# Kernel tuning notes

Hardware: AMD Instinct MI355X
Metric: run time of the kernel (lower is better)

Reference implementation:

```python
import jax, jax.numpy as jnp
import numpy as np

B, T, HID, MC, L, NCLS = 256, 128, 64, 30, 2, 100


def _flow(x, t, fW0, fb0, fW1, fb1, fW2, fb2, ftw):
    # Continuous affine coupling flow (stribor). x: [..., S, HID], t: [..., S, 1]
    hid = x.shape[-1]
    base = (jnp.arange(hid) < hid // 2).astype(x.dtype)  # ordered_0 mask
    for l in range(fW0.shape[0]):
        m = base if l % 2 == 0 else 1.0 - base
        z = x * m
        a = jnp.tanh(jnp.concatenate([z, t], -1) @ fW0[l] + fb0[l])
        a = jnp.tanh(a @ fW1[l] + fb1[l])
        ss = a @ fW2[l] + fb2[l]                      # [..., 2*hid]
        scale, shift = jnp.split(ss, 2, -1)
        t_scale, t_shift = jnp.split(jnp.tanh(t * ftw[l]), 2, -1)  # TimeTanh
        x = z + (1.0 - m) * (x * jnp.exp(scale * t_scale) + shift * t_shift)
    return x


def setup_inputs() -> dict:
    key = jax.random.key(0)
    ks = jax.random.split(key, 12)
    n = lambda k, s, sc=0.1: jax.random.normal(k, s, dtype=jnp.float32) * sc
    return {
        "times": jax.random.uniform(ks[0], (B, T, 1), dtype=jnp.float32),
        "marks": jax.random.randint(ks[1], (B, T, 1), 0, NCLS),
        "mask": jnp.ones((B, T, 1), jnp.float32),
        "u": jax.random.uniform(ks[2], (T, MC, 1), dtype=jnp.float32),
        "emb": n(ks[3], (NCLS, HID), 1.0),
        "fW0": n(ks[4], (L, HID + 1, HID)),
        "fb0": jnp.zeros((L, HID), jnp.float32),
        "fW1": n(ks[5], (L, HID, HID)),
        "fb1": jnp.zeros((L, HID), jnp.float32),
        "fW2": n(ks[6], (L, HID, 2 * HID)),
        "fb2": jnp.zeros((L, 2 * HID), jnp.float32),
        "ftw": n(ks[7], (L, 2 * HID), 1.0),
        "Wi": n(ks[8], (HID, 1)),
        "bi": jnp.zeros((1,), jnp.float32),
        "W_ih": n(ks[9], (4 * HID, 1 + HID)),
        "W_hh": n(ks[10], (4 * HID, HID)),
        "b_ih": jnp.zeros((4 * HID,), jnp.float32),
        "b_hh": jnp.zeros((4 * HID,), jnp.float32),
    }


def reference(times, marks, mask, u, emb, fW0, fb0, fW1, fb1, fW2, fb2, ftw,
              Wi, bi, W_ih, W_hh, b_ih, b_hh):
    Bn, Tn, _ = times.shape
    hid = emb.shape[1]
    mc = u.shape[1]
    marks_e = emb[marks[..., 0]]      # [B,T,hid]
    m1 = marks_e[:, 1]                # source uses marks[:, 1] every step (faithful)
    inten = lambda x: jax.nn.softplus(x @ Wi + bi)

    def step(carry, xs):
        h, c = carry                  # h,c: [B,hid]
        t, u_i = xs                   # t: [B,1], u_i: [mc,1]
        t3 = t[:, None, :]            # [B,1,1]
        ts = u_i[None] * t3           # [B,mc,1] MC time samples in [0,t)
        xb = jnp.broadcast_to(h[:, None, :], (Bn, mc, hid))
        path = _flow(xb, ts, fW0, fb0, fW1, fb1, fW2, fb2, ftw)   # [B,mc,hid]
        integral = inten(path).mean(1, keepdims=True) * t3        # [B,1,1]
        h2 = _flow(h[:, None, :], t3, fW0, fb0, fW1, fb1, fW2, fb2, ftw)  # [B,1,hid]
        lam = inten(h2)                                           # [B,1,1]
        gates = jnp.concatenate([t, m1], -1) @ W_ih.T + b_ih + h2[:, 0] @ W_hh.T + b_hh
        ig, fg, gg, og = jnp.split(gates, 4, -1)
        c_n = jax.nn.sigmoid(fg) * c + jax.nn.sigmoid(ig) * jnp.tanh(gg)
        h_n = jax.nn.sigmoid(og) * jnp.tanh(c_n)
        nll = -jnp.log(lam[:, 0]) + integral[:, 0]                # [B,1]
        return (h_n, c_n), (h2[:, 0], nll)

    h0 = jnp.zeros((Bn, hid), times.dtype)
    (_, _), (hidden, nll) = jax.lax.scan(step, (h0, h0), (jnp.swapaxes(times, 0, 1), u))
    hidden = jnp.swapaxes(hidden, 0, 1)                           # [B,T,hid]
    loss = (jnp.swapaxes(nll, 0, 1)[:, :, :] * mask[..., 0][..., None]).sum() / mask.sum()
    return loss, hidden
```

## Files before the change

kernel.cpp:

```cpp
#include <hip/hip_runtime.h>
#include <hip/hip_bf16.h>
#include <math.h>

#define Bn   256
#define Tn   128
#define HID  64
#define MCn  30

typedef __attribute__((ext_vector_type(8))) short bf16x8;
typedef __attribute__((ext_vector_type(4))) float f32x4;

__device__ __forceinline__ float rcp_(float x) { return __builtin_amdgcn_rcpf(x); }
__device__ __forceinline__ float tanhf_(float x) {
    float e = __expf(-2.0f * x);
    return __builtin_fmaf(2.0f, rcp_(1.0f + e), -1.0f);
}
__device__ __forceinline__ float sigmoidf_(float x) {
    return rcp_(1.0f + __expf(-x));
}
__device__ __forceinline__ float softplusf_(float z) {
    float e = __expf(-fabsf(z));
    return fmaxf(z, 0.0f) + __logf(1.0f + e);
}
__device__ __forceinline__ unsigned short f2b(float f) {
    union { float f; unsigned u; } v; v.f = f;
    unsigned r = v.u + 0x7FFF + ((v.u >> 16) & 1);
    return (unsigned short)(r >> 16);
}
__device__ __forceinline__ unsigned pk2(float a, float b) {
    union { __hip_bfloat162 h2; unsigned u; } cv;
    cv.h2 = __float22bfloat162_rn(make_float2(a, b));
    return cv.u;
}

extern "C" __global__ __launch_bounds__(256)
void prep_kernel(const int* __restrict__ marks, const float* __restrict__ mask,
                 const float* __restrict__ emb, const float* __restrict__ fW0,
                 const float* __restrict__ fW1, const float* __restrict__ fW2,
                 const float* __restrict__ fb0, const float* __restrict__ fb1,
                 const float* __restrict__ fb2, const float* __restrict__ ftw,
                 const float* __restrict__ Wi, const float* __restrict__ W_ih,
                 const float* __restrict__ W_hh,
                 const float* __restrict__ b_ih, const float* __restrict__ b_hh,
                 float* __restrict__ gc, float* __restrict__ invd,
                 float* __restrict__ parv, unsigned short* __restrict__ parwb,
                 float* __restrict__ seqw1T, float* __restrict__ seqw2T,
                 float* __restrict__ whh260)
{
    __shared__ float red[4];
    const int blk = blockIdx.x, tid = threadIdx.x;
    if (blk < Bn) {
        const int mark = marks[blk * Tn + 1];
        const float* er = emb + mark * HID;
        const float* wr = W_ih + tid * 65 + 1;
        float acc = b_ih[tid] + b_hh[tid];
        #pragma unroll
        for (int k = 0; k < HID; k++) acc += er[k] * wr[k];
        gc[blk * 256 + tid] = acc;
    } else if (blk == Bn) {
        float s = 0.f;
        for (int i = tid; i < Bn * Tn; i += 256) s += mask[i];
        #pragma unroll
        for (int off = 32; off >= 1; off >>= 1) s += __shfl_xor(s, off, 64);
        if ((tid & 63) == 0) red[tid >> 6] = s;
        __syncthreads();
        if (tid == 0) invd[0] = 1.0f / (red[0] + red[1] + red[2] + red[3]);
    } else if (blk == Bn + 1) {
        if (tid < 128) {
            int l = tid >> 6, m = tid & 63;
            parv[tid]       = fb0[tid];
            parv[128 + tid] = fW0[(l * 65 + 64) * 64 + m];
            parv[256 + tid] = fb1[tid];
            int act = 32 * (1 - l);
            parv[384 + tid] = fb2[l * 128 + act + (m & 31) + 64 * (m >> 5)];
        }
        if (tid < 64) {
            int l = tid >> 5, i2 = tid & 31, act = 32 * (1 - l);
            parv[512 + tid] = ftw[l * 128 + act + i2];
            parv[576 + tid] = ftw[l * 128 + 64 + act + i2];
            parv[640 + tid] = Wi[tid];
            parv[704 + tid] = 0.f;
        }
    } else if (blk == Bn + 2) {
        for (int i = tid; i < 5120; i += 256) {
            int k = i % 40, m = (i / 40) & 63, l = i / 2560;
            float v = (k < 32) ? fW0[(l * 65 + 32 * l + k) * 64 + m] : 0.f;
            parwb[i] = f2b(v);
        }
    } else if (blk == Bn + 3) {
        for (int i = tid; i < 9216; i += 256) {
            int k = i % 72, m = (i / 72) & 63, l = i / 4608;
            float v = (k < 64) ? fW1[(l * 64 + k) * 64 + m] : 0.f;
            parwb[5120 + i] = f2b(v);
        }
    } else if (blk == Bn + 4) {
        for (int i = tid; i < 9216; i += 256) {
            int k = i % 72, m = (i / 72) & 63, l = i / 4608;
            int act = 32 * (1 - l);
            float v = (k < 64) ? fW2[(l * 64 + k) * 128 + act + (m & 31) + 64 * (m >> 5)] : 0.f;
            parwb[14336 + i] = f2b(v);
        }
    } else if (blk == Bn + 5) {
        for (int i = tid; i < 8704; i += 256) {
            int k = i % 68, j = (i / 68) & 63, l = i / 4352;
            seqw1T[i] = (k < 64) ? fW1[(l * 64 + k) * 64 + j] : 0.f;
        }
    } else if (blk == Bn + 6) {
        for (int i = tid; i < 8704; i += 256) {
            int k = i % 68, j = (i / 68) & 63, l = i / 4352;
            int act = 32 * (1 - l);
            seqw2T[i] = (k < 64) ?
                fW2[(l * 64 + k) * 128 + act + (j & 31) + 64 * (j >> 5)] : 0.f;
        }
    } else {
        for (int i = tid; i < 16640; i += 256) {
            int j = i / 260, rem = i % 260, k = rem >> 2, r = rem & 3;
            whh260[i] = (k < 64) ? W_hh[(r * 64 + j) * 64 + k] : 0.f;
        }
    }
}

extern "C" __global__ __launch_bounds__(64, 1)
void seq_kernel(const float* __restrict__ times, const float* __restrict__ mask,
                const float* __restrict__ fW0, const float* __restrict__ fb0,
                const float* __restrict__ fb1, const float* __restrict__ fb2,
                const float* __restrict__ ftw, const float* __restrict__ Wi,
                const float* __restrict__ bi, const float* __restrict__ W_ih,
                const float* __restrict__ gc, const float* __restrict__ seqw1T,
                const float* __restrict__ invd,
                float* __restrict__ h_carry, float* __restrict__ out)
{
    const int j = threadIdx.x;
    const int b = blockIdx.x;

    extern __shared__ float smem[];
    float* w1l  = smem;
    float* w2l  = smem + 8704;
    float* whhl = smem + 17408;
    float* tl   = smem + 34048;
    float* ml   = smem + 34176;
    float* xl   = smem + 34304;
    float* al   = smem + 34368;
    float* ssl  = smem + 34432;

    {
        const float4* s = (const float4*)seqw1T;
        float4* d = (float4*)smem;
        for (int i = j; i < 8512; i += 64) d[i] = s[i];
    }
    tl[j] = times[b * Tn + j];       tl[j + 64] = times[b * Tn + 64 + j];
    ml[j] = mask[b * Tn + j];        ml[j + 64] = mask[b * Tn + 64 + j];

    float w0c[2][32], w0tc[2], b0c[2], b1c[2], b2c[2], ftsc[2], ftsh[2];
    #pragma unroll
    for (int l = 0; l < 2; l++) {
        #pragma unroll
        for (int kk = 0; kk < 32; kk++)
            w0c[l][kk] = fW0[(l * 65 + 32 * l + kk) * 64 + j];
        w0tc[l] = fW0[(l * 65 + 64) * 64 + j];
        b0c[l]  = fb0[l * 64 + j];
        b1c[l]  = fb1[l * 64 + j];
        const int act = 32 * (1 - l);
        b2c[l]  = fb2[l * 128 + act + (j & 31) + 64 * (j >> 5)];
        ftsc[l] = ftw[l * 128 + j];
        ftsh[l] = ftw[l * 128 + 64 + j];
    }
    const float wij = Wi[j];
    const float bi0 = bi[0];
    float wih0[4], gcr[4];
    #pragma unroll
    for (int r = 0; r < 4; r++) {
        wih0[r] = W_ih[(r * 64 + j) * 65];
        gcr[r]  = gc[b * 256 + r * 64 + j];
    }
    const float idn = invd[0];

    float h = 0.f, c = 0.f, nllacc = 0.f;
    for (int t = 0; t < Tn; t++) {
        const float tb = tl[t];
        float tscv[2], tshv[2];
        #pragma unroll
        for (int l = 0; l < 2; l++) {
            tscv[l] = tanhf_(tb * ftsc[l]);
            tshv[l] = tanhf_(tb * ftsh[l]);
        }
        h_carry[(b * Tn + t) * 64 + j] = h;
        float x = h;
        xl[j] = x;
        #pragma unroll
        for (int l = 0; l < 2; l++) {
            const int kb  = 32 * l;
            const int act = 32 * (1 - l);
            float p0 = b0c[l] + tb * w0tc[l], p1 = 0.f, p2 = 0.f, p3 = 0.f;
            {
                const float4* xv4 = (const float4*)(xl + kb);
                #pragma unroll
                for (int k4 = 0; k4 < 8; k4++) {
                    float4 xv = xv4[k4];
                    p0 += xv.x * w0c[l][4 * k4 + 0];
                    p1 += xv.y * w0c[l][4 * k4 + 1];
                    p2 += xv.z * w0c[l][4 * k4 + 2];
                    p3 += xv.w * w0c[l][4 * k4 + 3];
                }
            }
            al[j] = tanhf_((p0 + p1) + (p2 + p3));
            p0 = b1c[l]; p1 = p2 = p3 = 0.f;
            {
                const float4* av4 = (const float4*)al;
                const float*  wp  = w1l + (l * 64 + j) * 68;
                #pragma unroll
                for (int k4 = 0; k4 < 16; k4++) {
                    float4 av = av4[k4];
                    float4 wv = *(const float4*)(wp + 4 * k4);
                    p0 += av.x * wv.x;
                    p1 += av.y * wv.y;
                    p2 += av.z * wv.z;
                    p3 += av.w * wv.w;
                }
            }
            al[j] = tanhf_((p0 + p1) + (p2 + p3));
            p0 = b2c[l]; p1 = p2 = p3 = 0.f;
            {
                const float4* av4 = (const float4*)al;
                const float*  wp  = w2l + (l * 64 + j) * 68;
                #pragma unroll
                for (int k4 = 0; k4 < 16; k4++) {
                    float4 av = av4[k4];
                    float4 wv = *(const float4*)(wp + 4 * k4);
                    p0 += av.x * wv.x;
                    p1 += av.y * wv.y;
                    p2 += av.z * wv.z;
                    p3 += av.w * wv.w;
                }
            }
            ssl[j] = (p0 + p1) + (p2 + p3);
            const int idx = (j - act) & 31;
            const float scl = ssl[idx];
            const float shf = ssl[idx + 32];
            const float xa  = x * __expf(scl * tscv[l]) + shf * tshv[l];
            const bool active = (l == 0) ? (j >= 32) : (j < 32);
            x = active ? xa : x;
            xl[j] = x;
        }
        out[1 + (b * Tn + t) * 64 + j] = x;
        float v = x * wij;
        #pragma unroll
        for (int off = 32; off >= 1; off >>= 1) v += __shfl_xor(v, off, 64);
        nllacc += -__logf(softplusf_(v + bi0)) * ml[t];
        float g0 = gcr[0] + tb * wih0[0];
        float g1 = gcr[1] + tb * wih0[1];
        float g2 = gcr[2] + tb * wih0[2];
        float g3 = gcr[3] + tb * wih0[3];
        {
            const float*  wr_base = whhl + j * 260;
            const float4* hv4 = (const float4*)xl;
            #pragma unroll
            for (int k4 = 0; k4 < 16; k4++) {
                float4 hv = hv4[k4];
                const float* wr = wr_base + 16 * k4;
                float4 wa = *(const float4*)(wr);
                float4 wb = *(const float4*)(wr + 4);
                float4 wc = *(const float4*)(wr + 8);
                float4 wd = *(const float4*)(wr + 12);
                g0 += hv.x * wa.x; g1 += hv.x * wa.y; g2 += hv.x * wa.z; g3 += hv.x * wa.w;
                g0 += hv.y * wb.x; g1 += hv.y * wb.y; g2 += hv.y * wb.z; g3 += hv.y * wb.w;
                g0 += hv.z * wc.x; g1 += hv.z * wc.y; g2 += hv.z * wc.z; g3 += hv.z * wc.w;
                g0 += hv.w * wd.x; g1 += hv.w * wd.y; g2 += hv.w * wd.z; g3 += hv.w * wd.w;
            }
        }
        c = sigmoidf_(g1) * c + sigmoidf_(g0) * tanhf_(g2);
        h = sigmoidf_(g3) * tanhf_(c);
    }
    if (j == 0) atomicAdd(out, nllacc * idn);
}

extern "C" __global__ __launch_bounds__(256, 2)
void par_kernel(const float* __restrict__ times, const float* __restrict__ mask,
                const float* __restrict__ u, const float* __restrict__ bi,
                const float* __restrict__ invd, const float* __restrict__ parv,
                const unsigned short* __restrict__ parwb,
                const float* __restrict__ h_carry, float* __restrict__ pp)
{
    __shared__ __align__(16) unsigned short sact[128 * 72];
    __shared__ __align__(16) unsigned short sxk1[128 * 40];
    __shared__ __align__(16) unsigned short sx0b[4 * 40];
    __shared__ float pr[4];

    const int tid = threadIdx.x, lane = tid & 63, w = tid >> 6;
    const int quad = lane >> 4, l15 = lane & 15;

    const int q = blockIdx.x * 4 + w;
    const int t = q >> 8, b = q & 255;
    const float tb = times[b * Tn + t];
    const float* hrow = h_carry + (b * Tn + t) * 64;
    if (lane < 32) sx0b[w * 40 + lane] = f2b(hrow[lane]);

    float tsv[2], sclf[2];
    {
        const float base = tb * (1.0f / 30.0f) * invd[0] * mask[b * Tn + t];
        #pragma unroll
        for (int nt = 0; nt < 2; nt++) {
            int mc = nt * 16 + l15;
            bool val = (mc < 30);
            tsv[nt]  = val ? u[t * MCn + mc] * tb : 0.f;
            sclf[nt] = val ? base : 0.f;
        }
    }
    f32x4 xr[2][4];
    #pragma unroll
    for (int mt = 0; mt < 4; mt++) {
        f32x4 v = *(const f32x4*)(hrow + mt * 16 + quad * 4);
        xr[0][mt] = v; xr[1][mt] = v;
    }
    const int srow = w * 32;

    #pragma unroll
    for (int l = 0; l < 2; l++) {
        const unsigned short* wA1 = parwb + l * 2560;
        const unsigned short* wA2 = parwb + 5120 + l * 4608;
        const unsigned short* wA3 = parwb + 14336 + l * 4608;
        f32x4 c1[4][2];
        if (l == 0) {
            bf16x8 bb = *(const bf16x8*)(sx0b + w * 40 + quad * 8);
            #pragma unroll
            for (int mt = 0; mt < 4; mt++) {
                bf16x8 af = *(const bf16x8*)(wA1 + (mt * 16 + l15) * 40 + quad * 8);
                f32x4 z = {0.f, 0.f, 0.f, 0.f};
                c1[mt][0] = __builtin_amdgcn_mfma_f32_16x16x32_bf16(af, bb, z, 0, 0, 0);
                c1[mt][1] = c1[mt][0];
            }
        } else {
            bf16x8 bf[2];
            #pragma unroll
            for (int nt = 0; nt < 2; nt++)
                bf[nt] = *(const bf16x8*)(sxk1 + (srow + nt * 16 + l15) * 40 + quad * 8);
            #pragma unroll
            for (int mt = 0; mt < 4; mt++) {
                bf16x8 af = *(const bf16x8*)(wA1 + (mt * 16 + l15) * 40 + quad * 8);
                #pragma unroll
                for (int nt = 0; nt < 2; nt++) {
                    f32x4 z = {0.f, 0.f, 0.f, 0.f};
                    c1[mt][nt] = __builtin_amdgcn_mfma_f32_16x16x32_bf16(af, bf[nt], z, 0, 0, 0);
                }
            }
        }
        #pragma unroll
        for (int mt = 0; mt < 4; mt++) {
            f32x4 b0r = *(const f32x4*)(parv + 0   + l * 64 + mt * 16 + quad * 4);
            f32x4 w0r = *(const f32x4*)(parv + 128 + l * 64 + mt * 16 + quad * 4);
            #pragma unroll
            for (int nt = 0; nt < 2; nt++) {
                float v0 = tanhf_(c1[mt][nt][0] + b0r[0] + tsv[nt] * w0r[0]);
                float v1 = tanhf_(c1[mt][nt][1] + b0r[1] + tsv[nt] * w0r[1]);
                float v2 = tanhf_(c1[mt][nt][2] + b0r[2] + tsv[nt] * w0r[2]);
                float v3 = tanhf_(c1[mt][nt][3] + b0r[3] + tsv[nt] * w0r[3]);
                uint2 pk; pk.x = pk2(v0, v1); pk.y = pk2(v2, v3);
                *(uint2*)(sact + (srow + nt * 16 + l15) * 72 + mt * 16 + quad * 4) = pk;
            }
        }
        f32x4 cc[4][2];
        #pragma unroll
        for (int mt = 0; mt < 4; mt++)
            #pragma unroll
            for (int nt = 0; nt < 2; nt++) cc[mt][nt] = (f32x4){0.f, 0.f, 0.f, 0.f};
        #pragma unroll
        for (int kt = 0; kt < 2; kt++) {
            bf16x8 bf[2];
            #pragma unroll
            for (int nt = 0; nt < 2; nt++)
                bf[nt] = *(const bf16x8*)(sact + (srow + nt * 16 + l15) * 72 + kt * 32 + quad * 8);
            #pragma unroll
            for (int mt = 0; mt < 4; mt++) {
                bf16x8 af = *(const bf16x8*)(wA2 + (mt * 16 + l15) * 72 + kt * 32 + quad * 8);
                #pragma unroll
                for (int nt = 0; nt < 2; nt++)
                    cc[mt][nt] = __builtin_amdgcn_mfma_f32_16x16x32_bf16(af, bf[nt], cc[mt][nt], 0, 0, 0);
            }
        }
        #pragma unroll
        for (int mt = 0; mt < 4; mt++) {
            f32x4 b1r = *(const f32x4*)(parv + 256 + l * 64 + mt * 16 + quad * 4);
            #pragma unroll
            for (int nt = 0; nt < 2; nt++) {
                float v0 = tanhf_(cc[mt][nt][0] + b1r[0]);
                float v1 = tanhf_(cc[mt][nt][1] + b1r[1]);
                float v2 = tanhf_(cc[mt][nt][2] + b1r[2]);
                float v3 = tanhf_(cc[mt][nt][3] + b1r[3]);
                uint2 pk; pk.x = pk2(v0, v1); pk.y = pk2(v2, v3);
                *(uint2*)(sact + (srow + nt * 16 + l15) * 72 + mt * 16 + quad * 4) = pk;
            }
        }
        f32x4 ssf[4][2];
        #pragma unroll
        for (int mt = 0; mt < 4; mt++)
            #pragma unroll
            for (int nt = 0; nt < 2; nt++) ssf[mt][nt] = (f32x4){0.f, 0.f, 0.f, 0.f};
        #pragma unroll
        for (int kt = 0; kt < 2; kt++) {
            bf16x8 bf[2];
            #pragma unroll
            for (int nt = 0; nt < 2; nt++)
                bf[nt] = *(const bf16x8*)(sact + (srow + nt * 16 + l15) * 72 + kt * 32 + quad * 8);
            #pragma unroll
            for (int mt = 0; mt < 4; mt++) {
                bf16x8 af = *(const bf16x8*)(wA3 + (mt * 16 + l15) * 72 + kt * 32 + quad * 8);
                #pragma unroll
                for (int nt = 0; nt < 2; nt++)
                    ssf[mt][nt] = __builtin_amdgcn_mfma_f32_16x16x32_bf16(af, bf[nt], ssf[mt][nt], 0, 0, 0);
            }
        }
        #pragma unroll
        for (int mt2 = 0; mt2 < 2; mt2++) {
            f32x4 b2s = *(const f32x4*)(parv + 384 + l * 64 +      mt2 * 16 + quad * 4);
            f32x4 b2h = *(const f32x4*)(parv + 384 + l * 64 + 32 + mt2 * 16 + quad * 4);
            f32x4 fa  = *(const f32x4*)(parv + 512 + l * 32 + mt2 * 16 + quad * 4);
            f32x4 fb  = *(const f32x4*)(parv + 576 + l * 32 + mt2 * 16 + quad * 4);
            const int xm = (l == 0) ? (mt2 + 2) : mt2;
            #pragma unroll
            for (int nt = 0; nt < 2; nt++) {
                #pragma unroll
                for (int r = 0; r < 4; r++) {
                    float sc  = ssf[mt2][nt][r] + b2s[r];
                    float sh  = ssf[mt2 + 2][nt][r] + b2h[r];
                    float tsc = tanhf_(tsv[nt] * fa[r]);
                    float tsh = tanhf_(tsv[nt] * fb[r]);
                    float xv  = xr[nt][xm][r];
                    xr[nt][xm][r] = xv * __expf(sc * tsc) + sh * tsh;
                }
                if (l == 0) {
                    uint2 pk;
                    pk.x = pk2(xr[nt][xm][0], xr[nt][xm][1]);
                    pk.y = pk2(xr[nt][xm][2], xr[nt][xm][3]);
                    *(uint2*)(sxk1 + (srow + nt * 16 + l15) * 40 + mt2 * 16 + quad * 4) = pk;
                }
            }
        }
    }
    float contrib = 0.f;
    const float bi0 = bi[0];
    #pragma unroll
    for (int nt = 0; nt < 2; nt++) {
        float d0 = 0.f, d1 = 0.f;
        #pragma unroll
        for (int mt = 0; mt < 4; mt++) {
            f32x4 wi4 = *(const f32x4*)(parv + 640 + mt * 16 + quad * 4);
            d0 += xr[nt][mt][0] * wi4[0] + xr[nt][mt][2] * wi4[2];
            d1 += xr[nt][mt][1] * wi4[1] + xr[nt][mt][3] * wi4[3];
        }
        float d = d0 + d1;
        d += __shfl_xor(d, 16, 64);
        d += __shfl_xor(d, 32, 64);
        contrib += softplusf_(d + bi0) * sclf[nt];
    }
    if (quad != 0) contrib = 0.f;
    #pragma unroll
    for (int off = 1; off <= 8; off <<= 1) contrib += __shfl_xor(contrib, off, 64);
    if (l15 == 0 && quad == 0) pr[w] = contrib;
    __syncthreads();
    if (tid == 0) pp[blockIdx.x] = pr[0] + pr[1] + pr[2] + pr[3];
}

extern "C" __global__ __launch_bounds__(256)
void fin_kernel(const float* __restrict__ pp, float* __restrict__ out)
{
    __shared__ float r4[4];
    const int tid = threadIdx.x;
    float s = 0.f;
    for (int i = tid; i < (Bn * Tn) / 4; i += 256) s += pp[i];
    #pragma unroll
    for (int off = 32; off >= 1; off >>= 1) s += __shfl_xor(s, off, 64);
    if ((tid & 63) == 0) r4[tid >> 6] = s;
    __syncthreads();
    if (tid == 0) atomicAdd(out, r4[0] + r4[1] + r4[2] + r4[3]);
}

extern "C" void kernel_launch(void* const* d_in, const int* in_sizes, int n_in,
                              void* d_out, int out_size, void* d_ws, size_t ws_size,
                              hipStream_t stream)
{
    const float* times = (const float*)d_in[0];
    const int*   marks = (const int*)  d_in[1];
    const float* mask  = (const float*)d_in[2];
    const float* u     = (const float*)d_in[3];
    const float* emb   = (const float*)d_in[4];
    const float* fW0   = (const float*)d_in[5];
    const float* fb0   = (const float*)d_in[6];
    const float* fW1   = (const float*)d_in[7];
    const float* fb1   = (const float*)d_in[8];
    const float* fW2   = (const float*)d_in[9];
    const float* fb2   = (const float*)d_in[10];
    const float* ftw   = (const float*)d_in[11];
    const float* Wi    = (const float*)d_in[12];
    const float* bi    = (const float*)d_in[13];
    const float* W_ih  = (const float*)d_in[14];
    const float* W_hh  = (const float*)d_in[15];
    const float* b_ih  = (const float*)d_in[16];
    const float* b_hh  = (const float*)d_in[17];
    float* out = (float*)d_out;

    float* wsp     = (float*)d_ws;
    float* h_carry = wsp;
    float* gc      = h_carry + 2097152;
    float* invd    = gc + 65536;
    float* seqw1T  = invd + 4;
    float* seqw2T  = seqw1T + 8704;
    float* whh260  = seqw2T + 8704;
    float* parv    = whh260 + 16640;
    unsigned short* parwb = (unsigned short*)(parv + 768);
    float* pp      = (float*)(parwb + 23552);

    hipMemsetAsync(d_out, 0, sizeof(float), stream);

    const int SEQ_SMEM = 34496 * 4;
    hipFuncSetAttribute((const void*)seq_kernel,
                        hipFuncAttributeMaxDynamicSharedMemorySize, SEQ_SMEM);

    prep_kernel<<<Bn + 8, 256, 0, stream>>>(marks, mask, emb, fW0, fW1, fW2,
                                            fb0, fb1, fb2, ftw, Wi, W_ih, W_hh,
                                            b_ih, b_hh, gc, invd, parv, parwb,
                                            seqw1T, seqw2T, whh260);
    seq_kernel<<<Bn, 64, SEQ_SMEM, stream>>>(times, mask, fW0, fb0, fb1, fb2,
                                             ftw, Wi, bi, W_ih, gc, seqw1T,
                                             invd, h_carry, out);
    par_kernel<<<(Bn * Tn) / 4, 256, 0, stream>>>(
        times, mask, u, bi, invd, parv, parwb, h_carry, pp);
    fin_kernel<<<1, 256, 0, stream>>>(pp, out);
}
```

Baseline: 690.1 us.

## Fuse sequential LSTM scan with MC integral flow into one warp-specialized kernel

Merges seq_kernel, par_kernel and fin_kernel into one kernel of three waves per batch row. Wave 0 runs the serial flow+LSTM recurrence while waves 1-2 evaluate the Monte Carlo flow integral for the previous step's hidden state with MFMA, handing it over through a double-buffered shared hbuf. This removes the h_carry round trip through global memory, two kernel launches and the separate reduction, and hides the parallel work behind the serial chain. In exchange it adds a block barrier every timestep and runs the MC work on only 256 blocks instead of 8192.

```diff
diff --git a/kernel.cpp b/kernel.cpp
--- a/kernel.cpp
+++ b/kernel.cpp
@@ -120,18 +120,23 @@
     }
 }
 
-extern "C" __global__ __launch_bounds__(64, 1)
-void seq_kernel(const float* __restrict__ times, const float* __restrict__ mask,
-                const float* __restrict__ fW0, const float* __restrict__ fb0,
-                const float* __restrict__ fb1, const float* __restrict__ fb2,
-                const float* __restrict__ ftw, const float* __restrict__ Wi,
-                const float* __restrict__ bi, const float* __restrict__ W_ih,
-                const float* __restrict__ gc, const float* __restrict__ seqw1T,
-                const float* __restrict__ invd,
-                float* __restrict__ h_carry, float* __restrict__ out)
+extern "C" __global__ __launch_bounds__(192, 1)
+void fused_kernel(const float* __restrict__ times, const float* __restrict__ mask,
+                  const float* __restrict__ u,
+                  const float* __restrict__ fW0, const float* __restrict__ fb0,
+                  const float* __restrict__ fb1, const float* __restrict__ fb2,
+                  const float* __restrict__ ftw, const float* __restrict__ Wi,
+                  const float* __restrict__ bi, const float* __restrict__ W_ih,
+                  const float* __restrict__ gc, const float* __restrict__ seqw1T,
+                  const float* __restrict__ parv,
+                  const unsigned short* __restrict__ parwb,
+                  const float* __restrict__ invd, float* __restrict__ out)
 {
-    const int j = threadIdx.x;
-    const int b = blockIdx.x;
+    const int tid  = threadIdx.x;
+    const int lane = tid & 63;
+    const int w    = tid >> 6;
+    const int b    = blockIdx.x;
+    const int quad = lane >> 4, l15 = lane & 15;
 
     extern __shared__ float smem[];
     float* w1l  = smem;
@@ -142,336 +147,268 @@
     float* xl   = smem + 34304;
     float* al   = smem + 34368;
     float* ssl  = smem + 34432;
+    float* hbuf = smem + 34496;
+    float* pr   = smem + 34624;
+    unsigned short* csact = (unsigned short*)(smem + 34628);
+    unsigned short* csxk1 = csact + 2304;
+    unsigned short* csx0  = csxk1 + 1280;
 
     {
         const float4* s = (const float4*)seqw1T;
         float4* d = (float4*)smem;
-        for (int i = j; i < 8512; i += 64) d[i] = s[i];
+        for (int i = tid; i < 8512; i += 192) d[i] = s[i];
+        for (int i = tid; i < 128; i += 192) {
+            tl[i] = times[b * Tn + i];
+            ml[i] = mask[b * Tn + i];
+        }
     }
-    tl[j] = times[b * Tn + j];       tl[j + 64] = times[b * Tn + 64 + j];
-    ml[j] = mask[b * Tn + j];        ml[j + 64] = mask[b * Tn + 64 + j];
+
+    const float bi0 = bi[0];
+    const float idn = invd[0];
 
     float w0c[2][32], w0tc[2], b0c[2], b1c[2], b2c[2], ftsc[2], ftsh[2];
-    #pragma unroll
-    for (int l = 0; l < 2; l++) {
-        #pragma unroll
-        for (int kk = 0; kk < 32; kk++)
-            w0c[l][kk] = fW0[(l * 65 + 32 * l + kk) * 64 + j];
-        w0tc[l] = fW0[(l * 65 + 64) * 64 + j];
-        b0c[l]  = fb0[l * 64 + j];
-        b1c[l]  = fb1[l * 64 + j];
-        const int act = 32 * (1 - l);
-        b2c[l]  = fb2[l * 128 + act + (j & 31) + 64 * (j >> 5)];
-        ftsc[l] = ftw[l * 128 + j];
-        ftsh[l] = ftw[l * 128 + 64 + j];
-    }
-    const float wij = Wi[j];
-    const float bi0 = bi[0];
-    float wih0[4], gcr[4];
-    #pragma unroll
-    for (int r = 0; r < 4; r++) {
-        wih0[r] = W_ih[(r * 64 + j) * 65];
-        gcr[r]  = gc[b * 256 + r * 64 + j];
-    }
-    const float idn = invd[0];
-
+    float wih0[4], gcr[4], wij = 0.f;
     float h = 0.f, c = 0.f, nllacc = 0.f;
-    for (int t = 0; t < Tn; t++) {
-        const float tb = tl[t];
-        float tscv[2], tshv[2];
+    if (w == 0) {
         #pragma unroll
         for (int l = 0; l < 2; l++) {
-            tscv[l] = tanhf_(tb * ftsc[l]);
-            tshv[l] = tanhf_(tb * ftsh[l]);
-        }
-        h_carry[(b * Tn + t) * 64 + j] = h;
-        float x = h;
-        xl[j] = x;
+            #pragma unroll
+            for (int kk = 0; kk < 32; kk++)
+                w0c[l][kk] = fW0[(l * 65 + 32 * l + kk) * 64 + lane];
+            w0tc[l] = fW0[(l * 65 + 64) * 64 + lane];
+            b0c[l]  = fb0[l * 64 + lane];
+            b1c[l]  = fb1[l * 64 + lane];
+            const int act = 32 * (1 - l);
+            b2c[l]  = fb2[l * 128 + act + (lane & 31) + 64 * (lane >> 5)];
+            ftsc[l] = ftw[l * 128 + lane];
+            ftsh[l] = ftw[l * 128 + 64 + lane];
+        }
+        wij = Wi[lane];
         #pragma unroll
-        for (int l = 0; l < 2; l++) {
-            const int kb  = 32 * l;
-            const int act = 32 * (1 - l);
-            float p0 = b0c[l] + tb * w0tc[l], p1 = 0.f, p2 = 0.f, p3 = 0.f;
+        for (int r = 0; r < 4; r++) {
+            wih0[r] = W_ih[(r * 64 + lane) * 65];
+            gcr[r]  = gc[b * 256 + r * 64 + lane];
+        }
+    }
+    const int cw = w - 1;
+    unsigned short* myact = csact + cw * 1152;
+    unsigned short* myxk  = csxk1 + cw * 640;
+    unsigned short* myx0  = csx0  + cw * 40;
+    const int mc  = cw * 16 + l15;
+    const bool valmc = (w > 0) && (mc < MCn);
+    float wacc = 0.f;
+
+    __syncthreads();
+
+    for (int t = 0; t < Tn; t++) {
+        if (w == 0) hbuf[(t & 1) * 64 + lane] = h;
+        __syncthreads();
+
+        if (w == 0) {
+            const float tb = tl[t];
+            float tscv[2], tshv[2];
+            #pragma unroll
+            for (int l = 0; l < 2; l++) {
+                tscv[l] = tanhf_(tb * ftsc[l]);
+                tshv[l] = tanhf_(tb * ftsh[l]);
+            }
+            float x = h;
+            xl[lane] = x;
+            #pragma unroll
+            for (int l = 0; l < 2; l++) {
+                const int kb  = 32 * l;
+                const int act = 32 * (1 - l);
+                {
+                    float p0 = b0c[l] + tb * w0tc[l], p1 = 0.f, p2 = 0.f, p3 = 0.f;
+                    const float4* xv4 = (const float4*)(xl + kb);
+                    #pragma unroll
+                    for (int k4 = 0; k4 < 8; k4++) {
+                        float4 xv = xv4[k4];
+                        p0 += xv.x * w0c[l][4 * k4 + 0];
+                        p1 += xv.y * w0c[l][4 * k4 + 1];
+                        p2 += xv.z * w0c[l][4 * k4 + 2];
+                        p3 += xv.w * w0c[l][4 * k4 + 3];
+                    }
+                    al[lane] = tanhf_((p0 + p1) + (p2 + p3));
+                }
+                {
+                    float p0 = b1c[l], p1 = 0.f, p2 = 0.f, p3 = 0.f;
+                    const float4* av4 = (const float4*)al;
+                    const float*  wp  = w1l + (l * 64 + lane) * 68;
+                    #pragma unroll
+                    for (int k4 = 0; k4 < 16; k4++) {
+                        float4 av = av4[k4];
+                        float4 wv = *(const float4*)(wp + 4 * k4);
+                        p0 += av.x * wv.x; p1 += av.y * wv.y;
+                        p2 += av.z * wv.z; p3 += av.w * wv.w;
+                    }
+                    al[lane] = tanhf_((p0 + p1) + (p2 + p3));
+                }
+                {
+                    float p0 = b2c[l], p1 = 0.f, p2 = 0.f, p3 = 0.f;
+                    const float4* av4 = (const float4*)al;
+                    const float*  wp  = w2l + (l * 64 + lane) * 68;
+                    #pragma unroll
+                    for (int k4 = 0; k4 < 16; k4++) {
+                        float4 av = av4[k4];
+                        float4 wv = *(const float4*)(wp + 4 * k4);
+                        p0 += av.x * wv.x; p1 += av.y * wv.y;
+                        p2 += av.z * wv.z; p3 += av.w * wv.w;
+                    }
+                    ssl[lane] = (p0 + p1) + (p2 + p3);
+                }
+                const int idx = (lane - act) & 31;
+                const float scl = ssl[idx];
+                const float shf = ssl[idx + 32];
+                const float xa  = x * __expf(scl * tscv[l]) + shf * tshv[l];
+                const bool active = (l == 0) ? (lane >= 32) : (lane < 32);
+                x = active ? xa : x;
+                xl[lane] = x;
+            }
+            out[1 + (b * Tn + t) * 64 + lane] = x;
+            float v = x * wij;
+            #pragma unroll
+            for (int off = 32; off >= 1; off >>= 1) v += __shfl_xor(v, off, 64);
+            nllacc += -__logf(softplusf_(v + bi0)) * ml[t];
+            float g0 = gcr[0] + tb * wih0[0];
+            float g1 = gcr[1] + tb * wih0[1];
+            float g2 = gcr[2] + tb * wih0[2];
+            float g3 = gcr[3] + tb * wih0[3];
             {
-                const float4* xv4 = (const float4*)(xl + kb);
-                #pragma unroll
-                for (int k4 = 0; k4 < 8; k4++) {
-                    float4 xv = xv4[k4];
-                    p0 += xv.x * w0c[l][4 * k4 + 0];
-                    p1 += xv.y * w0c[l][4 * k4 + 1];
-                    p2 += xv.z * w0c[l][4 * k4 + 2];
-                    p3 += xv.w * w0c[l][4 * k4 + 3];
+                const float*  wr_base = whhl + lane * 260;
+                const float4* hv4 = (const float4*)xl;
+                #pragma unroll
+                for (int k4 = 0; k4 < 16; k4++) {
+                    float4 hv = hv4[k4];
+                    const float* wr = wr_base + 16 * k4;
+                    float4 wa = *(const float4*)(wr);
+                    float4 wb = *(const float4*)(wr + 4);
+                    float4 wc = *(const float4*)(wr + 8);
+                    float4 wd = *(const float4*)(wr + 12);
+                    g0 += hv.x * wa.x; g1 += hv.x * wa.y; g2 += hv.x * wa.z; g3 += hv.x * wa.w;
+                    g0 += hv.y * wb.x; g1 += hv.y * wb.y; g2 += hv.y * wb.z; g3 += hv.y * wb.w;
+                    g0 += hv.z * wc.x; g1 += hv.z * wc.y; g2 += hv.z * wc.z; g3 += hv.z * wc.w;
+                    g0 += hv.w * wd.x; g1 += hv.w * wd.y; g2 += hv.w * wd.z; g3 += hv.w * wd.w;
                 }
             }
-            al[j] = tanhf_((p0 + p1) + (p2 + p3));
-            p0 = b1c[l]; p1 = p2 = p3 = 0.f;
-            {
-                const float4* av4 = (const float4*)al;
-                const float*  wp  = w1l + (l * 64 + j) * 68;
-                #pragma unroll
-                for (int k4 = 0; k4 < 16; k4++) {
-                    float4 av = av4[k4];
-                    float4 wv = *(const float4*)(wp + 4 * k4);
-                    p0 += av.x * wv.x;
-                    p1 += av.y * wv.y;
-                    p2 += av.z * wv.z;
-                    p3 += av.w * wv.w;
+            c = sigmoidf_(g1) * c + sigmoidf_(g0) * tanhf_(g2);
+            h = sigmoidf_(g3) * tanhf_(c);
+        } else {
+            const float tb = tl[t];
+            const float ts   = valmc ? u[t * MCn + mc] * tb : 0.f;
+            const float sclf = valmc ? tb * (1.0f / 30.0f) * idn * ml[t] : 0.f;
+            const float* hb  = hbuf + (t & 1) * 64;
+            f32x4 xr[4];
+            #pragma unroll
+            for (int mt = 0; mt < 4; mt++)
+                xr[mt] = *(const f32x4*)(hb + mt * 16 + quad * 4);
+            if (lane < 32) myx0[lane] = f2b(hb[lane]);
+            #pragma unroll
+            for (int l = 0; l < 2; l++) {
+                const unsigned short* wA1 = parwb + l * 2560;
+                const unsigned short* wA2 = parwb + 5120 + l * 4608;
+                const unsigned short* wA3 = parwb + 14336 + l * 4608;
+                f32x4 c1[4];
+                {
+                    bf16x8 bfin = (l == 0) ? *(const bf16x8*)(myx0 + quad * 8)
+                                           : *(const bf16x8*)(myxk + l15 * 40 + quad * 8);
+                    #pragma unroll
+                    for (int mt = 0; mt < 4; mt++) {
+                        bf16x8 af = *(const bf16x8*)(wA1 + (mt * 16 + l15) * 40 + quad * 8);
+                        f32x4 z = {0.f, 0.f, 0.f, 0.f};
+                        c1[mt] = __builtin_amdgcn_mfma_f32_16x16x32_bf16(af, bfin, z, 0, 0, 0);
+                    }
+                }
+                #pragma unroll
+                for (int mt = 0; mt < 4; mt++) {
+                    f32x4 b0r = *(const f32x4*)(parv + 0   + l * 64 + mt * 16 + quad * 4);
+                    f32x4 w0r = *(const f32x4*)(parv + 128 + l * 64 + mt * 16 + quad * 4);
+                    float v0 = tanhf_(c1[mt][0] + b0r[0] + ts * w0r[0]);
+                    float v1 = tanhf_(c1[mt][1] + b0r[1] + ts * w0r[1]);
+                    float v2 = tanhf_(c1[mt][2] + b0r[2] + ts * w0r[2]);
+                    float v3 = tanhf_(c1[mt][3] + b0r[3] + ts * w0r[3]);
+                    uint2 pk; pk.x = pk2(v0, v1); pk.y = pk2(v2, v3);
+                    *(uint2*)(myact + l15 * 72 + mt * 16 + quad * 4) = pk;
+                }
+                f32x4 cc[4];
+                #pragma unroll
+                for (int mt = 0; mt < 4; mt++) cc[mt] = (f32x4){0.f, 0.f, 0.f, 0.f};
+                #pragma unroll
+                for (int kt = 0; kt < 2; kt++) {
+                    bf16x8 bfa = *(const bf16x8*)(myact + l15 * 72 + kt * 32 + quad * 8);
+                    #pragma unroll
+                    for (int mt = 0; mt < 4; mt++) {
+                        bf16x8 af = *(const bf16x8*)(wA2 + (mt * 16 + l15) * 72 + kt * 32 + quad * 8);
+                        cc[mt] = __builtin_amdgcn_mfma_f32_16x16x32_bf16(af, bfa, cc[mt], 0, 0, 0);
+                    }
+                }
+                #pragma unroll
+                for (int mt = 0; mt < 4; mt++) {
+                    f32x4 b1r = *(const f32x4*)(parv + 256 + l * 64 + mt * 16 + quad * 4);
+                    float v0 = tanhf_(cc[mt][0] + b1r[0]);
+                    float v1 = tanhf_(cc[mt][1] + b1r[1]);
+                    float v2 = tanhf_(cc[mt][2] + b1r[2]);
+                    float v3 = tanhf_(cc[mt][3] + b1r[3]);
+                    uint2 pk; pk.x = pk2(v0, v1); pk.y = pk2(v2, v3);
+                    *(uint2*)(myact + l15 * 72 + mt * 16 + quad * 4) = pk;
+                }
+                f32x4 ssf[4];
+                #pragma unroll
+                for (int mt = 0; mt < 4; mt++) ssf[mt] = (f32x4){0.f, 0.f, 0.f, 0.f};
+                #pragma unroll
+                for (int kt = 0; kt < 2; kt++) {
+                    bf16x8 bfa = *(const bf16x8*)(myact + l15 * 72 + kt * 32 + quad * 8);
+                    #pragma unroll
+                    for (int mt = 0; mt < 4; mt++) {
+                        bf16x8 af = *(const bf16x8*)(wA3 + (mt * 16 + l15) * 72 + kt * 32 + quad * 8);
+                        ssf[mt] = __builtin_amdgcn_mfma_f32_16x16x32_bf16(af, bfa, ssf[mt], 0, 0, 0);
+                    }
+                }
+                #pragma unroll
+                for (int mt2 = 0; mt2 < 2; mt2++) {
+                    f32x4 b2s = *(const f32x4*)(parv + 384 + l * 64 +      mt2 * 16 + quad * 4);
+                    f32x4 b2h = *(const f32x4*)(parv + 384 + l * 64 + 32 + mt2 * 16 + quad * 4);
+                    f32x4 fa  = *(const f32x4*)(parv + 512 + l * 32 + mt2 * 16 + quad * 4);
+                    f32x4 fb  = *(const f32x4*)(parv + 576 + l * 32 + mt2 * 16 + quad * 4);
+                    const int xm = (l == 0) ? (mt2 + 2) : mt2;
+                    #pragma unroll
+                    for (int r = 0; r < 4; r++) {
+                        float sc  = ssf[mt2][r] + b2s[r];
+                        float sh  = ssf[mt2 + 2][r] + b2h[r];
+                        float tsc = tanhf_(ts * fa[r]);
+                        float tsh = tanhf_(ts * fb[r]);
+                        xr[xm][r] = xr[xm][r] * __expf(sc * tsc) + sh * tsh;
+                    }
+                    if (l == 0) {
+                        uint2 pk;
+                        pk.x = pk2(xr[xm][0], xr[xm][1]);
+                        pk.y = pk2(xr[xm][2], xr[xm][3]);
+                        *(uint2*)(myxk + l15 * 40 + mt2 * 16 + quad * 4) = pk;
+                    }
                 }
             }
-            al[j] = tanhf_((p0 + p1) + (p2 + p3));
-            p0 = b2c[l]; p1 = p2 = p3 = 0.f;
-            {
-                const float4* av4 = (const float4*)al;
-                const float*  wp  = w2l + (l * 64 + j) * 68;
-                #pragma unroll
-                for (int k4 = 0; k4 < 16; k4++) {
-                    float4 av = av4[k4];
-                    float4 wv = *(const float4*)(wp + 4 * k4);
-                    p0 += av.x * wv.x;
-                    p1 += av.y * wv.y;
-                    p2 += av.z * wv.z;
-                    p3 += av.w * wv.w;
-                }
+            float d0 = 0.f, d1 = 0.f;
+            #pragma unroll
+            for (int mt = 0; mt < 4; mt++) {
+                f32x4 wi4 = *(const f32x4*)(parv + 640 + mt * 16 + quad * 4);
+                d0 += xr[mt][0] * wi4[0] + xr[mt][2] * wi4[2];
+                d1 += xr[mt][1] * wi4[1] + xr[mt][3] * wi4[3];
             }
-            ssl[j] = (p0 + p1) + (p2 + p3);
-            const int idx = (j - act) & 31;
-            const float scl = ssl[idx];
-            const float shf = ssl[idx + 32];
-            const float xa  = x * __expf(scl * tscv[l]) + shf * tshv[l];
-            const bool active = (l == 0) ? (j >= 32) : (j < 32);
-            x = active ? xa : x;
-            xl[j] = x;
-        }
-        out[1 + (b * Tn + t) * 64 + j] = x;
-        float v = x * wij;
+            float d = d0 + d1;
+            d += __shfl_xor(d, 16, 64);
+            d += __shfl_xor(d, 32, 64);
+            if (quad == 0) wacc += softplusf_(d + bi0) * sclf;
+        }
+    }
+    if (w == 0) {
+        if (lane == 0) pr[0] = nllacc * idn;
+    } else {
         #pragma unroll
-        for (int off = 32; off >= 1; off >>= 1) v += __shfl_xor(v, off, 64);
-        nllacc += -__logf(softplusf_(v + bi0)) * ml[t];
-        float g0 = gcr[0] + tb * wih0[0];
-        float g1 = gcr[1] + tb * wih0[1];
-        float g2 = gcr[2] + tb * wih0[2];
-        float g3 = gcr[3] + tb * wih0[3];
-        {
-            const float*  wr_base = whhl + j * 260;
-            const float4* hv4 = (const float4*)xl;
-            #pragma unroll
-            for (int k4 = 0; k4 < 16; k4++) {
-                float4 hv = hv4[k4];
-                const float* wr = wr_base + 16 * k4;
-                float4 wa = *(const float4*)(wr);
-                float4 wb = *(const float4*)(wr + 4);
-                float4 wc = *(const float4*)(wr + 8);
-                float4 wd = *(const float4*)(wr + 12);
-                g0 += hv.x * wa.x; g1 += hv.x * wa.y; g2 += hv.x * wa.z; g3 += hv.x * wa.w;
-                g0 += hv.y * wb.x; g1 += hv.y * wb.y; g2 += hv.y * wb.z; g3 += hv.y * wb.w;
-                g0 += hv.z * wc.x; g1 += hv.z * wc.y; g2 += hv.z * wc.z; g3 += hv.z * wc.w;
-                g0 += hv.w * wd.x; g1 += hv.w * wd.y; g2 += hv.w * wd.z; g3 += hv.w * wd.w;
-            }
-        }
-        c = sigmoidf_(g1) * c + sigmoidf_(g0) * tanhf_(g2);
-        h = sigmoidf_(g3) * tanhf_(c);
+        for (int off = 1; off <= 32; off <<= 1) wacc += __shfl_xor(wacc, off, 64);
+        if (lane == 0) pr[w] = wacc;
     }
-    if (j == 0) atomicAdd(out, nllacc * idn);
-}
-
-extern "C" __global__ __launch_bounds__(256, 2)
-void par_kernel(const float* __restrict__ times, const float* __restrict__ mask,
-                const float* __restrict__ u, const float* __restrict__ bi,
-                const float* __restrict__ invd, const float* __restrict__ parv,
-                const unsigned short* __restrict__ parwb,
-                const float* __restrict__ h_carry, float* __restrict__ pp)
-{
-    __shared__ __align__(16) unsigned short sact[128 * 72];
-    __shared__ __align__(16) unsigned short sxk1[128 * 40];
-    __shared__ __align__(16) unsigned short sx0b[4 * 40];
-    __shared__ float pr[4];
-
-    const int tid = threadIdx.x, lane = tid & 63, w = tid >> 6;
-    const int quad = lane >> 4, l15 = lane & 15;
-
-    const int q = blockIdx.x * 4 + w;
-    const int t = q >> 8, b = q & 255;
-    const float tb = times[b * Tn + t];
-    const float* hrow = h_carry + (b * Tn + t) * 64;
-    if (lane < 32) sx0b[w * 40 + lane] = f2b(hrow[lane]);
-
-    float tsv[2], sclf[2];
-    {
-        const float base = tb * (1.0f / 30.0f) * invd[0] * mask[b * Tn + t];
-        #pragma unroll
-        for (int nt = 0; nt < 2; nt++) {
-            int mc = nt * 16 + l15;
-            bool val = (mc < 30);
-            tsv[nt]  = val ? u[t * MCn + mc] * tb : 0.f;
-            sclf[nt] = val ? base : 0.f;
-        }
-    }
-    f32x4 xr[2][4];
-    #pragma unroll
-    for (int mt = 0; mt < 4; mt++) {
-        f32x4 v = *(const f32x4*)(hrow + mt * 16 + quad * 4);
-        xr[0][mt] = v; xr[1][mt] = v;
-    }
-    const int srow = w * 32;
-
-    #pragma unroll
-    for (int l = 0; l < 2; l++) {
-        const unsigned short* wA1 = parwb + l * 2560;
-        const unsigned short* wA2 = parwb + 5120 + l * 4608;
-        const unsigned short* wA3 = parwb + 14336 + l * 4608;
-        f32x4 c1[4][2];
-        if (l == 0) {
-            bf16x8 bb = *(const bf16x8*)(sx0b + w * 40 + quad * 8);
-            #pragma unroll
-            for (int mt = 0; mt < 4; mt++) {
-                bf16x8 af = *(const bf16x8*)(wA1 + (mt * 16 + l15) * 40 + quad * 8);
-                f32x4 z = {0.f, 0.f, 0.f, 0.f};
-                c1[mt][0] = __builtin_amdgcn_mfma_f32_16x16x32_bf16(af, bb, z, 0, 0, 0);
-                c1[mt][1] = c1[mt][0];
-            }
-        } else {
-            bf16x8 bf[2];
-            #pragma unroll
-            for (int nt = 0; nt < 2; nt++)
-                bf[nt] = *(const bf16x8*)(sxk1 + (srow + nt * 16 + l15) * 40 + quad * 8);
-            #pragma unroll
-            for (int mt = 0; mt < 4; mt++) {
-                bf16x8 af = *(const bf16x8*)(wA1 + (mt * 16 + l15) * 40 + quad * 8);
-                #pragma unroll
-                for (int nt = 0; nt < 2; nt++) {
-                    f32x4 z = {0.f, 0.f, 0.f, 0.f};
-                    c1[mt][nt] = __builtin_amdgcn_mfma_f32_16x16x32_bf16(af, bf[nt], z, 0, 0, 0);
-                }
-            }
-        }
-        #pragma unroll
-        for (int mt = 0; mt < 4; mt++) {
-            f32x4 b0r = *(const f32x4*)(parv + 0   + l * 64 + mt * 16 + quad * 4);
-            f32x4 w0r = *(const f32x4*)(parv + 128 + l * 64 + mt * 16 + quad * 4);
-            #pragma unroll
-            for (int nt = 0; nt < 2; nt++) {
-                float v0 = tanhf_(c1[mt][nt][0] + b0r[0] + tsv[nt] * w0r[0]);
-                float v1 = tanhf_(c1[mt][nt][1] + b0r[1] + tsv[nt] * w0r[1]);
-                float v2 = tanhf_(c1[mt][nt][2] + b0r[2] + tsv[nt] * w0r[2]);
-                float v3 = tanhf_(c1[mt][nt][3] + b0r[3] + tsv[nt] * w0r[3]);
-                uint2 pk; pk.x = pk2(v0, v1); pk.y = pk2(v2, v3);
-                *(uint2*)(sact + (srow + nt * 16 + l15) * 72 + mt * 16 + quad * 4) = pk;
-            }
-        }
-        f32x4 cc[4][2];
-        #pragma unroll
-        for (int mt = 0; mt < 4; mt++)
-            #pragma unroll
-            for (int nt = 0; nt < 2; nt++) cc[mt][nt] = (f32x4){0.f, 0.f, 0.f, 0.f};
-        #pragma unroll
-        for (int kt = 0; kt < 2; kt++) {
-            bf16x8 bf[2];
-            #pragma unroll
-            for (int nt = 0; nt < 2; nt++)
-                bf[nt] = *(const bf16x8*)(sact + (srow + nt * 16 + l15) * 72 + kt * 32 + quad * 8);
-            #pragma unroll
-            for (int mt = 0; mt < 4; mt++) {
-                bf16x8 af = *(const bf16x8*)(wA2 + (mt * 16 + l15) * 72 + kt * 32 + quad * 8);
-                #pragma unroll
-                for (int nt = 0; nt < 2; nt++)
-                    cc[mt][nt] = __builtin_amdgcn_mfma_f32_16x16x32_bf16(af, bf[nt], cc[mt][nt], 0, 0, 0);
-            }
-        }
-        #pragma unroll
-        for (int mt = 0; mt < 4; mt++) {
-            f32x4 b1r = *(const f32x4*)(parv + 256 + l * 64 + mt * 16 + quad * 4);
-            #pragma unroll
-            for (int nt = 0; nt < 2; nt++) {
-                float v0 = tanhf_(cc[mt][nt][0] + b1r[0]);
-                float v1 = tanhf_(cc[mt][nt][1] + b1r[1]);
-                float v2 = tanhf_(cc[mt][nt][2] + b1r[2]);
-                float v3 = tanhf_(cc[mt][nt][3] + b1r[3]);
-                uint2 pk; pk.x = pk2(v0, v1); pk.y = pk2(v2, v3);
-                *(uint2*)(sact + (srow + nt * 16 + l15) * 72 + mt * 16 + quad * 4) = pk;
-            }
-        }
-        f32x4 ssf[4][2];
-        #pragma unroll
-        for (int mt = 0; mt < 4; mt++)
-            #pragma unroll
-            for (int nt = 0; nt < 2; nt++) ssf[mt][nt] = (f32x4){0.f, 0.f, 0.f, 0.f};
-        #pragma unroll
-        for (int kt = 0; kt < 2; kt++) {
-            bf16x8 bf[2];
-            #pragma unroll
-            for (int nt = 0; nt < 2; nt++)
-                bf[nt] = *(const bf16x8*)(sact + (srow + nt * 16 + l15) * 72 + kt * 32 + quad * 8);
-            #pragma unroll
-            for (int mt = 0; mt < 4; mt++) {
-                bf16x8 af = *(const bf16x8*)(wA3 + (mt * 16 + l15) * 72 + kt * 32 + quad * 8);
-                #pragma unroll
-                for (int nt = 0; nt < 2; nt++)
-                    ssf[mt][nt] = __builtin_amdgcn_mfma_f32_16x16x32_bf16(af, bf[nt], ssf[mt][nt], 0, 0, 0);
-            }
-        }
-        #pragma unroll
-        for (int mt2 = 0; mt2 < 2; mt2++) {
-            f32x4 b2s = *(const f32x4*)(parv + 384 + l * 64 +      mt2 * 16 + quad * 4);
-            f32x4 b2h = *(const f32x4*)(parv + 384 + l * 64 + 32 + mt2 * 16 + quad * 4);
-            f32x4 fa  = *(const f32x4*)(parv + 512 + l * 32 + mt2 * 16 + quad * 4);
-            f32x4 fb  = *(const f32x4*)(parv + 576 + l * 32 + mt2 * 16 + quad * 4);
-            const int xm = (l == 0) ? (mt2 + 2) : mt2;
-            #pragma unroll
-            for (int nt = 0; nt < 2; nt++) {
-                #pragma unroll
-                for (int r = 0; r < 4; r++) {
-                    float sc  = ssf[mt2][nt][r] + b2s[r];
-                    float sh  = ssf[mt2 + 2][nt][r] + b2h[r];
-                    float tsc = tanhf_(tsv[nt] * fa[r]);
-                    float tsh = tanhf_(tsv[nt] * fb[r]);
-                    float xv  = xr[nt][xm][r];
-                    xr[nt][xm][r] = xv * __expf(sc * tsc) + sh * tsh;
-                }
-                if (l == 0) {
-                    uint2 pk;
-                    pk.x = pk2(xr[nt][xm][0], xr[nt][xm][1]);
-                    pk.y = pk2(xr[nt][xm][2], xr[nt][xm][3]);
-                    *(uint2*)(sxk1 + (srow + nt * 16 + l15) * 40 + mt2 * 16 + quad * 4) = pk;
-                }
-            }
-        }
-    }
-    float contrib = 0.f;
-    const float bi0 = bi[0];
-    #pragma unroll
-    for (int nt = 0; nt < 2; nt++) {
-        float d0 = 0.f, d1 = 0.f;
-        #pragma unroll
-        for (int mt = 0; mt < 4; mt++) {
-            f32x4 wi4 = *(const f32x4*)(parv + 640 + mt * 16 + quad * 4);
-            d0 += xr[nt][mt][0] * wi4[0] + xr[nt][mt][2] * wi4[2];
-            d1 += xr[nt][mt][1] * wi4[1] + xr[nt][mt][3] * wi4[3];
-        }
-        float d = d0 + d1;
-        d += __shfl_xor(d, 16, 64);
-        d += __shfl_xor(d, 32, 64);
-        contrib += softplusf_(d + bi0) * sclf[nt];
-    }
-    if (quad != 0) contrib = 0.f;
-    #pragma unroll
-    for (int off = 1; off <= 8; off <<= 1) contrib += __shfl_xor(contrib, off, 64);
-    if (l15 == 0 && quad == 0) pr[w] = contrib;
     __syncthreads();
-    if (tid == 0) pp[blockIdx.x] = pr[0] + pr[1] + pr[2] + pr[3];
-}
-
-extern "C" __global__ __launch_bounds__(256)
-void fin_kernel(const float* __restrict__ pp, float* __restrict__ out)
-{
-    __shared__ float r4[4];
-    const int tid = threadIdx.x;
-    float s = 0.f;
-    for (int i = tid; i < (Bn * Tn) / 4; i += 256) s += pp[i];
-    #pragma unroll
-    for (int off = 32; off >= 1; off >>= 1) s += __shfl_xor(s, off, 64);
-    if ((tid & 63) == 0) r4[tid >> 6] = s;
-    __syncthreads();
-    if (tid == 0) atomicAdd(out, r4[0] + r4[1] + r4[2] + r4[3]);
+    if (tid == 0) atomicAdd(out, pr[0] + pr[1] + pr[2]);
 }
 
 extern "C" void kernel_launch(void* const* d_in, const int* in_sizes, int n_in,
@@ -499,30 +436,26 @@
     float* out = (float*)d_out;
 
     float* wsp     = (float*)d_ws;
-    float* h_carry = wsp;
-    float* gc      = h_carry + 2097152;
+    float* gc      = wsp;
     float* invd    = gc + 65536;
     float* seqw1T  = invd + 4;
     float* seqw2T  = seqw1T + 8704;
     float* whh260  = seqw2T + 8704;
     float* parv    = whh260 + 16640;
     unsigned short* parwb = (unsigned short*)(parv + 768);
-    float* pp      = (float*)(parwb + 23552);
 
     hipMemsetAsync(d_out, 0, sizeof(float), stream);
 
-    const int SEQ_SMEM = 34496 * 4;
-    hipFuncSetAttribute((const void*)seq_kernel,
-                        hipFuncAttributeMaxDynamicSharedMemorySize, SEQ_SMEM);
+    const int FUSED_SMEM = 34628 * 4 + 7328;
+    hipFuncSetAttribute((const void*)fused_kernel,
+                        hipFuncAttributeMaxDynamicSharedMemorySize, FUSED_SMEM);
 
     prep_kernel<<<Bn + 8, 256, 0, stream>>>(marks, mask, emb, fW0, fW1, fW2,
                                             fb0, fb1, fb2, ftw, Wi, W_ih, W_hh,
                                             b_ih, b_hh, gc, invd, parv, parwb,
                                             seqw1T, seqw2T, whh260);
-    seq_kernel<<<Bn, 64, SEQ_SMEM, stream>>>(times, mask, fW0, fb0, fb1, fb2,
-                                             ftw, Wi, bi, W_ih, gc, seqw1T,
-                                             invd, h_carry, out);
-    par_kernel<<<(Bn * Tn) / 4, 256, 0, stream>>>(
-        times, mask, u, bi, invd, parv, parwb, h_carry, pp);
-    fin_kernel<<<1, 256, 0, stream>>>(pp, out);
-}
+    fused_kernel<<<Bn, 192, FUSED_SMEM, stream>>>(times, mask, u, fW0, fb0,
+                                                  fb1, fb2, ftw, Wi, bi, W_ih,
+                                                  gc, seqw1T, parv, parwb,
+                                                  invd, out);
+}
```

After: 616.7 us. 1.12x faster.
